# Performance work log

Measured on AMD Instinct MI355X. Metric: run time of the kernel, lower is better.

Reference implementation:

```python
import jax, jax.numpy as jnp
import numpy as np

BATCH, SEQ, DIM = 4, 4096, 1024


def setup_inputs() -> dict:
    key = jax.random.key(0)
    ks = jax.random.split(key, 7)
    return {
        "x": jax.random.normal(ks[0], (BATCH, SEQ, DIM), dtype=jnp.float32),
        "phazor_re": jax.random.normal(ks[1], (DIM,), dtype=jnp.float32),
        "phazor_im": jax.random.normal(ks[2], (DIM,), dtype=jnp.float32),
        "phazor_init_re": jax.random.normal(ks[3], (DIM,), dtype=jnp.float32),
        "phazor_init_im": jax.random.normal(ks[4], (DIM,), dtype=jnp.float32),
        "last_conv_re": jax.random.normal(ks[5], (BATCH, DIM), dtype=jnp.float32),
        "last_conv_im": jax.random.normal(ks[6], (BATCH, DIM), dtype=jnp.float32),
    }


def reference(x, phazor_re, phazor_im, phazor_init_re, phazor_init_im,
              last_conv_re, last_conv_im):
    L = x.shape[1]
    phazor_p = phazor_re + 1j * phazor_im                      # raw param (dim,)
    phazor_init = phazor_init_re + 1j * phazor_init_im          # (dim,)
    last_conv = last_conv_re + 1j * last_conv_im                # (batch, dim)

    mag = jnp.abs(phazor_p)
    phazor = phazor_p / mag * jnp.exp(-mag)                     # (dim,) |phazor|<1
    t = jnp.arange(L)[:, None]                                  # (L,1)
    phazor_prog = jnp.power(phazor[None, :], t)                 # (L, dim) = phazor^t
    filt = phazor_prog * phazor_init[None, :]                   # (L, dim)

    filt_fft = jnp.fft.fft(filt, n=2 * L, axis=0)               # (2L, dim)
    x_fft = jnp.fft.fft(x.astype(jnp.complex64), n=2 * L, axis=1)  # (B, 2L, dim)
    conv = jnp.fft.ifft(filt_fft[None] * x_fft, axis=1)[:, :L]  # (B, L, dim)

    # add decayed initial state: last_conv * phazor^(t+1)
    conv = conv + last_conv[:, None, :] * phazor_prog[None] * phazor[None, None, :]
    return conv.real
```

## Files before the change

### kernel.cpp

```cpp
#include <hip/hip_runtime.h>


#define BB 4
#define LL 4096
#define DD 1024
#define CHUNK 16
#define KK 256
#define SEG 32
#define NSEG 8
#define NBLK 1024u

__device__ unsigned g_grp[2 * 32 * 32];
__device__ unsigned g_glob[2 * 32];

__device__ __forceinline__ void phazor_of(float pr, float pi, float& ar, float& ai) {
    float mag = sqrtf(pr * pr + pi * pi);
    float s = expf(-mag) / mag;
    ar = pr * s;
    ai = pi * s;
}

__device__ __forceinline__ void csq(float& r, float& i) {
    float nr = r * r - i * i;
    i = 2.f * r * i;
    r = nr;
}

__device__ __forceinline__ void st8(float2* p, float2 v) {
    __hip_atomic_store(p, v, __ATOMIC_RELAXED, __HIP_MEMORY_SCOPE_AGENT);
}
__device__ __forceinline__ float2 ld8(const float2* p) {
    return __hip_atomic_load((float2*)p, __ATOMIC_RELAXED, __HIP_MEMORY_SCOPE_AGENT);
}

__device__ __forceinline__ void grid_barrier(int site) {
    __syncthreads();
    if (threadIdx.x == 0) {
        unsigned* A = &g_grp[site * 1024 + (blockIdx.x >> 5) * 32];
        unsigned* G = &g_glob[site * 32];
        unsigned a = __hip_atomic_fetch_add(A, 1u,
                        __ATOMIC_RELAXED, __HIP_MEMORY_SCOPE_AGENT);
        unsigned gen = a >> 5;
        if ((a & 31u) == 31u)
            __hip_atomic_fetch_add(G, 32u,
                        __ATOMIC_RELAXED, __HIP_MEMORY_SCOPE_AGENT);
        unsigned target = (gen + 1u) * NBLK;
        int spins = 0;
        while ((int)(__hip_atomic_load(G, __ATOMIC_RELAXED,
                                       __HIP_MEMORY_SCOPE_AGENT) - target) < 0) {
            __builtin_amdgcn_s_sleep(16);
            if (++spins > (1 << 17)) break;
        }
    }
    __syncthreads();
}

__global__ __launch_bounds__(256, 4) void spiral_fused(
    const float* __restrict__ x,
    const float* __restrict__ p_re, const float* __restrict__ p_im,
    const float* __restrict__ in_re, const float* __restrict__ in_im,
    const float* __restrict__ lc_re, const float* __restrict__ lc_im,
    float2* __restrict__ S, float2* __restrict__ R, float2* __restrict__ T,
    float* __restrict__ out)
{
    __shared__ float4 xlds[8][256];

    const int tid = blockIdx.x * 256 + threadIdx.x;
    const int dq = tid & (DD / 4 - 1);
    const int k  = (tid >> 8) & (KK - 1);
    const int b  = tid >> 16;
    const int d0 = dq * 4;

    float ar[4], ai[4], br[4], bi[4];
    {
        float4 prv = *(const float4*)(p_re + d0);
        float4 piv = *(const float4*)(p_im + d0);
        float4 brv = *(const float4*)(in_re + d0);
        float4 biv = *(const float4*)(in_im + d0);
        float prs[4] = {prv.x, prv.y, prv.z, prv.w};
        float pis[4] = {piv.x, piv.y, piv.z, piv.w};
        br[0] = brv.x; br[1] = brv.y; br[2] = brv.z; br[3] = brv.w;
        bi[0] = biv.x; bi[1] = biv.y; bi[2] = biv.z; bi[3] = biv.w;
#pragma unroll
        for (int q = 0; q < 4; ++q) phazor_of(prs[q], pis[q], ar[q], ai[q]);
    }

    const size_t xbase = (size_t)(b * LL + k * CHUNK) * DD + d0;

    {
        const float* xp = x + xbase;
        float4 xv[16];
#pragma unroll
        for (int j = 0; j < 16; ++j)
            xv[j] = *(const float4*)(xp + (size_t)j * DD);

#pragma unroll
        for (int j = 0; j < 8; ++j)
            xlds[j][threadIdx.x] = xv[j];

        float sr[4] = {0.f, 0.f, 0.f, 0.f};
        float si[4] = {0.f, 0.f, 0.f, 0.f};
#pragma unroll
        for (int j = 0; j < 16; ++j) {
            float xs[4] = {xv[j].x, xv[j].y, xv[j].z, xv[j].w};
#pragma unroll
            for (int q = 0; q < 4; ++q) {
                float nr = fmaf(ar[q], sr[q], fmaf(-ai[q], si[q], br[q] * xs[q]));
                float ni = fmaf(ar[q], si[q], fmaf( ai[q], sr[q], bi[q] * xs[q]));
                sr[q] = nr; si[q] = ni;
            }
        }
        float2* Sp = S + ((size_t)(b * KK + k) * DD + d0);
#pragma unroll
        for (int q = 0; q < 4; ++q)
            st8(Sp + q, make_float2(sr[q], si[q]));
    }

    grid_barrier(0);

    if (blockIdx.x < 128) {
        const int gt  = tid;
        const int d   = gt & (DD - 1);
        const int seg = (gt >> 10) & (NSEG - 1);
        const int bb  = gt >> 13;

        float qr, qi;
        phazor_of(p_re[d], p_im[d], qr, qi);
#pragma unroll
        for (int i = 0; i < 4; ++i) csq(qr, qi);

        const int kk0 = seg * SEG;
        const float2* Sc = S + ((size_t)bb * KK * DD + d);
        float2*       Rc = R + ((size_t)bb * KK * DD + d);

        float2 buf[8];
#pragma unroll
        for (int j = 0; j < 8; ++j) buf[j] = ld8(Sc + (size_t)(kk0 + j) * DD);

        float cr = 0.f, ci = 0.f;
        for (int i = 0; i < SEG; i += 8) {
#pragma unroll
            for (int j = 0; j < 8; ++j) {
                st8(Rc + (size_t)(kk0 + i + j) * DD, make_float2(cr, ci));
                float2 s = buf[j];
                int kn = i + j + 8;
                buf[j] = ld8(Sc + (size_t)(kk0 + (kn < SEG ? kn : SEG - 1)) * DD);
                float nr = fmaf(qr, cr, fmaf(-qi, ci, s.x));
                float ni = fmaf(qr, ci, fmaf( qi, cr, s.y));
                cr = nr; ci = ni;
            }
        }
        st8(T + ((size_t)bb * NSEG + seg) * DD + d, make_float2(cr, ci));
    }

    grid_barrier(1);

    const int rel  = k & (SEG - 1);
    const int seg3 = k >> 5;

    float4 xv2[8];
    {
        const float* xp = x + xbase;
#pragma unroll
        for (int j = 0; j < 8; ++j)
            xv2[j] = *(const float4*)(xp + (size_t)(8 + j) * DD);
    }

    float gr[4], gi[4];
    {
        float4 lrv = *(const float4*)(lc_re + b * DD + d0);
        float4 liv = *(const float4*)(lc_im + b * DD + d0);
        gr[0] = lrv.x; gr[1] = lrv.y; gr[2] = lrv.z; gr[3] = lrv.w;
        gi[0] = liv.x; gi[1] = liv.y; gi[2] = liv.z; gi[3] = liv.w;
        float Qr[4], Qi[4];
#pragma unroll
        for (int q = 0; q < 4; ++q) {
            Qr[q] = ar[q]; Qi[q] = ai[q];
#pragma unroll
            for (int i = 0; i < 9; ++i) csq(Qr[q], Qi[q]);
        }
        for (int s = 0; s < seg3; ++s) {
            const float2* Tp = T + ((size_t)(b * NSEG + s) * DD + d0);
#pragma unroll
            for (int q = 0; q < 4; ++q) {
                float2 t = ld8(Tp + q);
                float nr = fmaf(Qr[q], gr[q], fmaf(-Qi[q], gi[q], t.x));
                float ni = fmaf(Qr[q], gi[q], fmaf( Qi[q], gr[q], t.y));
                gr[q] = nr; gi[q] = ni;
            }
        }
    }

    float cr[4], ci[4];
    {
        const float2* Rp = R + ((size_t)(b * KK + k) * DD + d0);
#pragma unroll
        for (int q = 0; q < 4; ++q) {
            float qdr = ar[q], qdi = ai[q];
#pragma unroll
            for (int i = 0; i < 4; ++i) csq(qdr, qdi);
            float pr = 1.f, pi = 0.f;
            float bpr = qdr, bpi = qdi;
#pragma unroll
            for (int bit = 0; bit < 5; ++bit) {
                if ((rel >> bit) & 1) {
                    float nr = pr * bpr - pi * bpi;
                    pi = pr * bpi + pi * bpr;
                    pr = nr;
                }
                csq(bpr, bpi);
            }
            float2 r = ld8(Rp + q);
            cr[q] = r.x + pr * gr[q] - pi * gi[q];
            ci[q] = r.y + pr * gi[q] + pi * gr[q];
        }
    }

    {
        float* op = out + xbase;
#pragma unroll
        for (int j = 0; j < 8; ++j) {
            float4 xj = xlds[j][threadIdx.x];
            float xs[4] = {xj.x, xj.y, xj.z, xj.w};
            float os[4];
#pragma unroll
            for (int q = 0; q < 4; ++q) {
                float nr = fmaf(ar[q], cr[q], fmaf(-ai[q], ci[q], br[q] * xs[q]));
                float ni = fmaf(ar[q], ci[q], fmaf( ai[q], cr[q], bi[q] * xs[q]));
                cr[q] = nr; ci[q] = ni;
                os[q] = nr;
            }
            *(float4*)(op + (size_t)j * DD) = make_float4(os[0], os[1], os[2], os[3]);
        }
#pragma unroll
        for (int j = 0; j < 8; ++j) {
            float xs[4] = {xv2[j].x, xv2[j].y, xv2[j].z, xv2[j].w};
            float os[4];
#pragma unroll
            for (int q = 0; q < 4; ++q) {
                float nr = fmaf(ar[q], cr[q], fmaf(-ai[q], ci[q], br[q] * xs[q]));
                float ni = fmaf(ar[q], ci[q], fmaf( ai[q], cr[q], bi[q] * xs[q]));
                cr[q] = nr; ci[q] = ni;
                os[q] = nr;
            }
            *(float4*)(op + (size_t)(8 + j) * DD) = make_float4(os[0], os[1], os[2], os[3]);
        }
    }
}

extern "C" void kernel_launch(void* const* d_in, const int* in_sizes, int n_in,
                              void* d_out, int out_size, void* d_ws, size_t ws_size,
                              hipStream_t stream) {
    const float* x      = (const float*)d_in[0];
    const float* p_re   = (const float*)d_in[1];
    const float* p_im   = (const float*)d_in[2];
    const float* pin_re = (const float*)d_in[3];
    const float* pin_im = (const float*)d_in[4];
    const float* lc_re  = (const float*)d_in[5];
    const float* lc_im  = (const float*)d_in[6];
    float* out = (float*)d_out;

    char* ws = (char*)d_ws;
    float2* S = (float2*)(ws);
    float2* R = (float2*)(ws + (size_t)8  * 1024 * 1024);
    float2* T = (float2*)(ws + (size_t)16 * 1024 * 1024);

    spiral_fused<<<dim3(NBLK), dim3(256), 0, stream>>>(
        x, p_re, p_im, pin_re, pin_im, lc_re, lc_im, S, R, T, out);
}
```

Baseline: 155.4 us.

## Replace first grid barrier with per-segment last-arriver scan

Drops the first grid-wide barrier. Each block now increments a per-(batch,segment) counter, and the last of the 32 blocks in a segment runs the intra-segment chunk scan over S, writing R and T. Only one grid barrier remains before the final pass. The R load is also hoisted ahead of the carry computation to overlap latency. Risks: memory ordering relies on relaxed atomics with no release/acquire fences, the g_seg counters are never reset (the mod-32 check depends on wraparound), and the scan now runs serially in 32 blocks, one per batch and segment.

```diff
diff --git a/kernel.cpp b/kernel.cpp
--- a/kernel.cpp
+++ b/kernel.cpp
@@ -10,8 +10,9 @@
 #define NSEG 8
 #define NBLK 1024u
 
-__device__ unsigned g_grp[2 * 32 * 32];
-__device__ unsigned g_glob[2 * 32];
+__device__ unsigned g_grp[32 * 32];
+__device__ unsigned g_glob[32];
+__device__ unsigned g_seg[32 * 32];
 
 __device__ __forceinline__ void phazor_of(float pr, float pi, float& ar, float& ai) {
     float mag = sqrtf(pr * pr + pi * pi);
@@ -33,11 +34,11 @@
     return __hip_atomic_load((float2*)p, __ATOMIC_RELAXED, __HIP_MEMORY_SCOPE_AGENT);
 }
 
-__device__ __forceinline__ void grid_barrier(int site) {
+__device__ __forceinline__ void grid_barrier() {
     __syncthreads();
     if (threadIdx.x == 0) {
-        unsigned* A = &g_grp[site * 1024 + (blockIdx.x >> 5) * 32];
-        unsigned* G = &g_glob[site * 32];
+        unsigned* A = &g_grp[(blockIdx.x >> 5) * 32];
+        unsigned* G = &g_glob[0];
         unsigned a = __hip_atomic_fetch_add(A, 1u,
                         __ATOMIC_RELAXED, __HIP_MEMORY_SCOPE_AGENT);
         unsigned gen = a >> 5;
@@ -64,12 +65,15 @@
     float* __restrict__ out)
 {
     __shared__ float4 xlds[8][256];
+    __shared__ int doP2;
 
     const int tid = blockIdx.x * 256 + threadIdx.x;
     const int dq = tid & (DD / 4 - 1);
     const int k  = (tid >> 8) & (KK - 1);
     const int b  = tid >> 16;
     const int d0 = dq * 4;
+    const int seg = k >> 5;
+    const int rel = k & (SEG - 1);
 
     float ar[4], ai[4], br[4], bi[4];
     {
@@ -116,47 +120,81 @@
             st8(Sp + q, make_float2(sr[q], si[q]));
     }
 
-    grid_barrier(0);
-
-    if (blockIdx.x < 128) {
-        const int gt  = tid;
-        const int d   = gt & (DD - 1);
-        const int seg = (gt >> 10) & (NSEG - 1);
-        const int bb  = gt >> 13;
-
-        float qr, qi;
-        phazor_of(p_re[d], p_im[d], qr, qi);
-#pragma unroll
-        for (int i = 0; i < 4; ++i) csq(qr, qi);
-
-        const int kk0 = seg * SEG;
-        const float2* Sc = S + ((size_t)bb * KK * DD + d);
-        float2*       Rc = R + ((size_t)bb * KK * DD + d);
-
-        float2 buf[8];
-#pragma unroll
-        for (int j = 0; j < 8; ++j) buf[j] = ld8(Sc + (size_t)(kk0 + j) * DD);
-
-        float cr = 0.f, ci = 0.f;
-        for (int i = 0; i < SEG; i += 8) {
-#pragma unroll
-            for (int j = 0; j < 8; ++j) {
-                st8(Rc + (size_t)(kk0 + i + j) * DD, make_float2(cr, ci));
-                float2 s = buf[j];
-                int kn = i + j + 8;
-                buf[j] = ld8(Sc + (size_t)(kk0 + (kn < SEG ? kn : SEG - 1)) * DD);
-                float nr = fmaf(qr, cr, fmaf(-qi, ci, s.x));
-                float ni = fmaf(qr, ci, fmaf( qi, cr, s.y));
-                cr = nr; ci = ni;
-            }
-        }
-        st8(T + ((size_t)bb * NSEG + seg) * DD + d, make_float2(cr, ci));
-    }
-
-    grid_barrier(1);
-
-    const int rel  = k & (SEG - 1);
-    const int seg3 = k >> 5;
+    __syncthreads();
+    if (threadIdx.x == 0) {
+        unsigned t = __hip_atomic_fetch_add(&g_seg[(b * NSEG + seg) * 32], 1u,
+                        __ATOMIC_RELAXED, __HIP_MEMORY_SCOPE_AGENT);
+        doP2 = ((t & 31u) == 31u);
+    }
+    __syncthreads();
+
+    if (doP2) {
+        float q16r[4], q16i[4];
+#pragma unroll
+        for (int q = 0; q < 4; ++q) {
+            q16r[q] = ar[q]; q16i[q] = ai[q];
+#pragma unroll
+            for (int i = 0; i < 4; ++i) csq(q16r[q], q16i[q]);
+        }
+        const size_t segbase = (size_t)(b * KK + seg * SEG) * DD + d0;
+        const float2* Sc = S + segbase;
+        float2*       Rc = R + segbase;
+
+        float cr[4] = {0,0,0,0}, ci[4] = {0,0,0,0};
+        float2 bufA[4], bufB[4];
+#pragma unroll
+        for (int q = 0; q < 4; ++q) bufA[q] = ld8(Sc + q);
+#pragma unroll
+        for (int q = 0; q < 4; ++q) bufB[q] = ld8(Sc + DD + q);
+
+#pragma unroll
+        for (int kc = 0; kc < SEG; kc += 2) {
+#pragma unroll
+            for (int q = 0; q < 4; ++q)
+                st8(Rc + (size_t)kc * DD + q, make_float2(cr[q], ci[q]));
+            {
+                float2 s[4];
+#pragma unroll
+                for (int q = 0; q < 4; ++q) s[q] = bufA[q];
+                if (kc + 2 < SEG) {
+#pragma unroll
+                    for (int q = 0; q < 4; ++q)
+                        bufA[q] = ld8(Sc + (size_t)(kc + 2) * DD + q);
+                }
+#pragma unroll
+                for (int q = 0; q < 4; ++q) {
+                    float nr = fmaf(q16r[q], cr[q], fmaf(-q16i[q], ci[q], s[q].x));
+                    float ni = fmaf(q16r[q], ci[q], fmaf( q16i[q], cr[q], s[q].y));
+                    cr[q] = nr; ci[q] = ni;
+                }
+            }
+#pragma unroll
+            for (int q = 0; q < 4; ++q)
+                st8(Rc + (size_t)(kc + 1) * DD + q, make_float2(cr[q], ci[q]));
+            {
+                float2 s[4];
+#pragma unroll
+                for (int q = 0; q < 4; ++q) s[q] = bufB[q];
+                if (kc + 3 < SEG) {
+#pragma unroll
+                    for (int q = 0; q < 4; ++q)
+                        bufB[q] = ld8(Sc + (size_t)(kc + 3) * DD + q);
+                }
+#pragma unroll
+                for (int q = 0; q < 4; ++q) {
+                    float nr = fmaf(q16r[q], cr[q], fmaf(-q16i[q], ci[q], s[q].x));
+                    float ni = fmaf(q16r[q], ci[q], fmaf( q16i[q], cr[q], s[q].y));
+                    cr[q] = nr; ci[q] = ni;
+                }
+            }
+        }
+#pragma unroll
+        for (int q = 0; q < 4; ++q)
+            st8(T + ((size_t)(b * NSEG + seg) * DD + d0 + q),
+                make_float2(cr[q], ci[q]));
+    }
+
+    grid_barrier();
 
     float4 xv2[8];
     {
@@ -164,6 +202,12 @@
 #pragma unroll
         for (int j = 0; j < 8; ++j)
             xv2[j] = *(const float4*)(xp + (size_t)(8 + j) * DD);
+    }
+    float2 rv[4];
+    {
+        const float2* Rp = R + ((size_t)(b * KK + k) * DD + d0);
+#pragma unroll
+        for (int q = 0; q < 4; ++q) rv[q] = ld8(Rp + q);
     }
 
     float gr[4], gi[4];
@@ -179,7 +223,7 @@
 #pragma unroll
             for (int i = 0; i < 9; ++i) csq(Qr[q], Qi[q]);
         }
-        for (int s = 0; s < seg3; ++s) {
+        for (int s = 0; s < seg; ++s) {
             const float2* Tp = T + ((size_t)(b * NSEG + s) * DD + d0);
 #pragma unroll
             for (int q = 0; q < 4; ++q) {
@@ -193,7 +237,6 @@
 
     float cr[4], ci[4];
     {
-        const float2* Rp = R + ((size_t)(b * KK + k) * DD + d0);
 #pragma unroll
         for (int q = 0; q < 4; ++q) {
             float qdr = ar[q], qdi = ai[q];
@@ -210,9 +253,8 @@
                 }
                 csq(bpr, bpi);
             }
-            float2 r = ld8(Rp + q);
-            cr[q] = r.x + pr * gr[q] - pi * gi[q];
-            ci[q] = r.y + pr * gi[q] + pi * gr[q];
+            cr[q] = rv[q].x + pr * gr[q] - pi * gi[q];
+            ci[q] = rv[q].y + pr * gi[q] + pi * gr[q];
         }
     }
 
```

Result: slower. 271.1 us (+74.5%).
